# Kernel tuning notes

Measured on AMD Instinct MI355X. Metric: run time of the kernel, lower is better.

## Reference

```python
import jax, jax.numpy as jnp
import numpy as np

B, S, D, H = 2, 4096, 512, 8
DK = D // H  # 64

def setup_inputs() -> dict:
    key = jax.random.key(0)
    k1, k2, k3, k4 = jax.random.split(key, 4)
    return {
        "queries": jax.random.normal(k1, (B, S, D), dtype=jnp.float32),
        "keys": jax.random.normal(k2, (B, S, D), dtype=jnp.float32),
        "values": jax.random.normal(k3, (B, S, D), dtype=jnp.float32),
        "W_o": jax.random.normal(k4, (D, D), dtype=jnp.float32) * (1.0 / np.sqrt(D)),
        "b_o": jnp.zeros((D,), dtype=jnp.float32),
    }

def reference(queries, keys, values, W_o, b_o):
    b_s, nq, _ = queries.shape
    nk = keys.shape[1]
    # split heads: (b, s, h, dk) -> (b, h, s, dk)
    q = queries.reshape(b_s, nq, H, DK).transpose(0, 2, 1, 3)
    k = keys.reshape(b_s, nk, H, DK).transpose(0, 2, 1, 3)
    v = values.reshape(b_s, nk, H, DK).transpose(0, 2, 1, 3)
    # full (nq, nk) attention matrix, scaled by sqrt(d_k)
    att = jnp.einsum("bhqd,bhkd->bhqk", q, k) / np.sqrt(DK).astype(np.float32)
    att = jax.nn.softmax(att, axis=-1)  # dropout is identity at inference
    out = jnp.einsum("bhqk,bhkd->bhqd", att, v)
    out = out.transpose(0, 2, 1, 3).reshape(b_s, nq, H * DK)
    return out @ W_o + b_o
```

## Files before the change

kernel.cpp:

```cpp
#include <hip/hip_runtime.h>
#include <hip/hip_bf16.h>

#define Bn 2
#define Sn 4096
#define Dn 512
#define Hn 8

typedef _Float16 f16x8 __attribute__((ext_vector_type(8)));
typedef __fp16 fp16x2 __attribute__((ext_vector_type(2)));
typedef float f32x16 __attribute__((ext_vector_type(16)));
typedef unsigned uint2v __attribute__((ext_vector_type(2)));

#if __has_builtin(__builtin_amdgcn_global_load_lds)
#define HAS_GLL 1
typedef const __attribute__((address_space(1))) unsigned int* gas1_t;
typedef __attribute__((address_space(3))) unsigned int* las3_t;
static __device__ __forceinline__ void ld_lds16(const void* g, void* l) {
    __builtin_amdgcn_global_load_lds((gas1_t)g, (las3_t)l, 16, 0, 0);
}
#else
#define HAS_GLL 0
#endif

static __device__ __forceinline__ unsigned pkh(float a, float b) {
    union { fp16x2 h; unsigned u; } r;
    r.h = __builtin_amdgcn_cvt_pkrtz(a, b);
    return r.u;
}

static __device__ __forceinline__ f16x8 xchg2(unsigned g0x, unsigned g0y,
                                              unsigned g1x, unsigned g1y, int hi) {
    union { unsigned u[4]; f16x8 v; } f;
#if __has_builtin(__builtin_amdgcn_permlane32_swap)
    uint2v rx = __builtin_amdgcn_permlane32_swap(g0x, g1x, false, false);
    uint2v ry = __builtin_amdgcn_permlane32_swap(g0y, g1y, false, false);
    f.u[0] = rx.x; f.u[1] = ry.x; f.u[2] = rx.y; f.u[3] = ry.y;
#else
    int sx = hi ? (int)g0x : (int)g1x;
    int sy = hi ? (int)g0y : (int)g1y;
    int rx = __shfl_xor(sx, 32);
    int ry = __shfl_xor(sy, 32);
    unsigned ox = hi ? g1x : g0x;
    unsigned oy = hi ? g1y : g0y;
    f.u[0] = hi ? (unsigned)rx : ox;
    f.u[1] = hi ? (unsigned)ry : oy;
    f.u[2] = hi ? ox : (unsigned)rx;
    f.u[3] = hi ? oy : (unsigned)ry;
#endif
    return f.v;
}

__global__ __launch_bounds__(256) void prep_kernel(
    const float* __restrict__ K, const float* __restrict__ V, const float* __restrict__ W,
    unsigned short* __restrict__ Kb, unsigned short* __restrict__ Vb,
    unsigned short* __restrict__ Wb) {
    const int vb = blockIdx.x;
    const int tid = threadIdx.x;
    if (vb < 1024) {
        const int kt = vb & 63, bh = vb >> 6;
        const int b = bh >> 3, h = bh & 7;
        unsigned short* dst = Kb + ((size_t)bh * 64 + kt) * 4096;
#pragma unroll
        for (int i = 0; i < 2; ++i) {
            int c = tid + i * 256;
            int f = c >> 6, ln = c & 63;
            int ktile = f >> 2, ks = f & 3;
            int row = ktile * 32 + (ln & 31);
            int dk = ks * 16 + (ln >> 5) * 8;
            const float* src = K + ((size_t)(b * Sn + kt * 64 + row)) * Dn + h * 64 + dk;
            float4 a0 = *(const float4*)src;
            float4 a1 = *(const float4*)(src + 4);
            uint4 o;
            o.x = pkh(a0.x, a0.y); o.y = pkh(a0.z, a0.w);
            o.z = pkh(a1.x, a1.y); o.w = pkh(a1.z, a1.w);
            *(uint4*)(dst + c * 8) = o;
        }
    } else if (vb < 2048) {
        const int u = vb - 1024;
        const int kt = u & 63, bh = u >> 6;
        const int b = bh >> 3, h = bh & 7;
        unsigned short* dst = Vb + ((size_t)bh * 64 + kt) * 4096;
#pragma unroll
        for (int i = 0; i < 2; ++i) {
            int c = tid + i * 256;
            int f = c >> 6, ln = c & 63;
            int dt = f >> 2, ks = f & 3;
            int dk = dt * 32 + (ln & 31);
            int key0 = ks * 16 + (ln >> 5) * 8;
            const float* src = V + ((size_t)(b * Sn + kt * 64 + key0)) * Dn + h * 64 + dk;
            uint4 o;
            o.x = pkh(src[0 * Dn], src[1 * Dn]);
            o.y = pkh(src[2 * Dn], src[3 * Dn]);
            o.z = pkh(src[4 * Dn], src[5 * Dn]);
            o.w = pkh(src[6 * Dn], src[7 * Dn]);
            *(uint4*)(dst + c * 8) = o;
        }
    } else {
        int c = (vb - 2048) * 256 + tid;
        int ln = c & 63, f = c >> 6;
        int ntile = f >> 5, ks = f & 31;
        int n = ntile * 32 + (ln & 31);
        int k0 = ks * 16 + (ln >> 5) * 8;
        uint4 o;
        o.x = pkh(W[(size_t)(k0 + 0) * Dn + n], W[(size_t)(k0 + 1) * Dn + n]);
        o.y = pkh(W[(size_t)(k0 + 2) * Dn + n], W[(size_t)(k0 + 3) * Dn + n]);
        o.z = pkh(W[(size_t)(k0 + 4) * Dn + n], W[(size_t)(k0 + 5) * Dn + n]);
        o.w = pkh(W[(size_t)(k0 + 6) * Dn + n], W[(size_t)(k0 + 7) * Dn + n]);
        *(uint4*)(Wb + c * 8) = o;
    }
}

__global__ __launch_bounds__(512, 2) void attn_kernel(
    const float* __restrict__ Q,
    const unsigned short* __restrict__ Kb,
    const unsigned short* __restrict__ Vb,
    unsigned short* __restrict__ ObA) {
    __shared__ __align__(16) unsigned short KV[32768];

    const int id = blockIdx.x + (blockIdx.y << 5);
    const int qt = (id >> 3) & 31;
    const int bh = (id & 7) + ((id >> 8) << 3);
    const int b = bh >> 3, h = bh & 7;
    const int tid = threadIdx.x;
    const int wg = tid >> 6;
    const int kg = wg >> 1;
    const int qs = wg & 1;
    const int lane = tid & 63;
    const int q = lane & 31;
    const int hi = lane >> 5;
    const float cexp = 0.18033688f;

    f16x8 qf0[4], qf1[4];
    {
        const float* qp0 = Q + ((size_t)(b * Sn + qt * 128 + qs * 64 + q)) * Dn + h * 64 + hi * 8;
        const float* qp1 = qp0 + (size_t)32 * Dn;
#pragma unroll
        for (int ks = 0; ks < 4; ++ks) {
            float4 a0 = *(const float4*)(qp0 + ks * 16);
            float4 a1 = *(const float4*)(qp0 + ks * 16 + 4);
            union { unsigned u[4]; f16x8 v; } f;
            f.u[0] = pkh(a0.x * cexp, a0.y * cexp);
            f.u[1] = pkh(a0.z * cexp, a0.w * cexp);
            f.u[2] = pkh(a1.x * cexp, a1.y * cexp);
            f.u[3] = pkh(a1.z * cexp, a1.w * cexp);
            qf0[ks] = f.v;
            a0 = *(const float4*)(qp1 + ks * 16);
            a1 = *(const float4*)(qp1 + ks * 16 + 4);
            f.u[0] = pkh(a0.x * cexp, a0.y * cexp);
            f.u[1] = pkh(a0.z * cexp, a0.w * cexp);
            f.u[2] = pkh(a1.x * cexp, a1.y * cexp);
            f.u[3] = pkh(a1.z * cexp, a1.w * cexp);
            qf1[ks] = f.v;
        }
    }

    f32x16 zf;
#pragma unroll
    for (int r = 0; r < 16; ++r) zf[r] = 0.f;
    f32x16 oacc[2][2];
    oacc[0][0] = zf; oacc[0][1] = zf; oacc[1][0] = zf; oacc[1][1] = zf;
    float l0_ = 0.f, l1_ = 0.f;

    const size_t bhbase = (size_t)bh * 64 * 4096;

#if HAS_GLL
#define STAGE(itx, bb) { \
    const int t64 = kg * 16 + ((itx) >> 1); \
    const int lohi = (itx) & 1; \
    unsigned short* dst = &KV[(bb) * 16384 + kg * 4096]; \
    if (qs == 0) { \
        const unsigned short* sp = Kb + bhbase + (size_t)t64 * 4096 + lohi * 2048 + lane * 8; \
        ld_lds16(sp, dst); ld_lds16(sp + 512, dst + 512); \
        ld_lds16(sp + 1024, dst + 1024); ld_lds16(sp + 1536, dst + 1536); \
    } else { \
        const unsigned short* sp = Vb + bhbase + (size_t)t64 * 4096 + lohi * 1024 + lane * 8; \
        unsigned short* dv = dst + 2048; \
        ld_lds16(sp, dv); ld_lds16(sp + 512, dv + 512); \
        ld_lds16(sp + 2048, dv + 1024); ld_lds16(sp + 2560, dv + 1536); \
    } }
#else
#define STAGE(itx, bb) { \
    const int t64 = kg * 16 + ((itx) >> 1); \
    const int lohi = (itx) & 1; \
    unsigned short* dst = &KV[(bb) * 16384 + kg * 4096]; \
    if (qs == 0) { \
        const unsigned short* sp = Kb + bhbase + (size_t)t64 * 4096 + lohi * 2048 + lane * 8; \
        uint4 a0 = *(const uint4*)(sp); uint4 a1 = *(const uint4*)(sp + 512); \
        uint4 a2 = *(const uint4*)(sp + 1024); uint4 a3 = *(const uint4*)(sp + 1536); \
        *(uint4*)&dst[lane * 8] = a0; *(uint4*)&dst[512 + lane * 8] = a1; \
        *(uint4*)&dst[1024 + lane * 8] = a2; *(uint4*)&dst[1536 + lane * 8] = a3; \
    } else { \
        const unsigned short* sp = Vb + bhbase + (size_t)t64 * 4096 + lohi * 1024 + lane * 8; \
        unsigned short* dv = dst + 2048; \
        uint4 a0 = *(const uint4*)(sp); uint4 a1 = *(const uint4*)(sp + 512); \
        uint4 a2 = *(const uint4*)(sp + 2048); uint4 a3 = *(const uint4*)(sp + 2560); \
        *(uint4*)&dv[lane * 8] = a0; *(uint4*)&dv[512 + lane * 8] = a1; \
        *(uint4*)&dv[1024 + lane * 8] = a2; *(uint4*)&dv[1536 + lane * 8] = a3; \
    } }
#endif

    STAGE(0, 0);

    for (int it = 0; it < 32; ++it) {
        __syncthreads();
        const unsigned short* Kbuf = &KV[(it & 1) * 16384 + kg * 4096];
        const unsigned short* Vbuf = Kbuf + 2048;
        if (it < 31) STAGE(it + 1, (it + 1) & 1);

        f32x16 sa0, sa1;
        {
            f16x8 kf = *(const f16x8*)&Kbuf[0 * 512 + lane * 8];
            sa0 = __builtin_amdgcn_mfma_f32_32x32x16_f16(kf, qf0[0], zf, 0, 0, 0);
            sa1 = __builtin_amdgcn_mfma_f32_32x32x16_f16(kf, qf1[0], zf, 0, 0, 0);
#pragma unroll
            for (int ks = 1; ks < 4; ++ks) {
                kf = *(const f16x8*)&Kbuf[ks * 512 + lane * 8];
                sa0 = __builtin_amdgcn_mfma_f32_32x32x16_f16(kf, qf0[ks], sa0, 0, 0, 0);
                sa1 = __builtin_amdgcn_mfma_f32_32x32x16_f16(kf, qf1[ks], sa1, 0, 0, 0);
            }
        }
        unsigned u0[8], u1[8];
        float s0 = 0.f, s1 = 0.f;
#pragma unroll
        for (int j = 0; j < 8; ++j) {
            float ea = __builtin_amdgcn_exp2f(sa0[2 * j]);
            float eb = __builtin_amdgcn_exp2f(sa0[2 * j + 1]);
            s0 += ea + eb;
            u0[j] = pkh(ea, eb);
        }
#pragma unroll
        for (int j = 0; j < 8; ++j) {
            float ea = __builtin_amdgcn_exp2f(sa1[2 * j]);
            float eb = __builtin_amdgcn_exp2f(sa1[2 * j + 1]);
            s1 += ea + eb;
            u1[j] = pkh(ea, eb);
        }
        l0_ += s0; l1_ += s1;

#pragma unroll
        for (int ks2 = 0; ks2 < 2; ++ks2) {
            f16x8 pb0 = xchg2(u0[4 * ks2 + 0], u0[4 * ks2 + 1], u0[4 * ks2 + 2], u0[4 * ks2 + 3], hi);
            f16x8 pb1 = xchg2(u1[4 * ks2 + 0], u1[4 * ks2 + 1], u1[4 * ks2 + 2], u1[4 * ks2 + 3], hi);
            f16x8 va0 = *(const f16x8*)&Vbuf[ks2 * 512 + lane * 8];
            f16x8 va1 = *(const f16x8*)&Vbuf[1024 + ks2 * 512 + lane * 8];
            oacc[0][0] = __builtin_amdgcn_mfma_f32_32x32x16_f16(va0, pb0, oacc[0][0], 0, 0, 0);
            oacc[0][1] = __builtin_amdgcn_mfma_f32_32x32x16_f16(va1, pb0, oacc[0][1], 0, 0, 0);
            oacc[1][0] = __builtin_amdgcn_mfma_f32_32x32x16_f16(va0, pb1, oacc[1][0], 0, 0, 0);
            oacc[1][1] = __builtin_amdgcn_mfma_f32_32x32x16_f16(va1, pb1, oacc[1][1], 0, 0, 0);
        }
    }

    __syncthreads();
    float* red = (float*)KV;
#pragma unroll
    for (int t = 0; t < 2; ++t) {
        if (kg != 0) {
            float* rp = red + (qs * 3 + (kg - 1)) * 2048;
#pragma unroll
            for (int dt = 0; dt < 2; ++dt)
#pragma unroll
                for (int g = 0; g < 4; ++g) {
                    float4 v;
                    v.x = oacc[t][dt][g * 4 + 0];
                    v.y = oacc[t][dt][g * 4 + 1];
                    v.z = oacc[t][dt][g * 4 + 2];
                    v.w = oacc[t][dt][g * 4 + 3];
                    *(float4*)&rp[(dt * 4 + g) * 256 + lane * 4] = v;
                }
            red[12288 + (qs * 3 + (kg - 1)) * 64 + lane] = t ? l1_ : l0_;
        }
        __syncthreads();
        if (kg == 0) {
#pragma unroll
            for (int slot = 0; slot < 3; ++slot) {
                float* rp = red + (qs * 3 + slot) * 2048;
#pragma unroll
                for (int dt = 0; dt < 2; ++dt)
#pragma unroll
                    for (int g = 0; g < 4; ++g) {
                        float4 v = *(const float4*)&rp[(dt * 4 + g) * 256 + lane * 4];
                        oacc[t][dt][g * 4 + 0] += v.x;
                        oacc[t][dt][g * 4 + 1] += v.y;
                        oacc[t][dt][g * 4 + 2] += v.z;
                        oacc[t][dt][g * 4 + 3] += v.w;
                    }
                float addl = red[12288 + (qs * 3 + slot) * 64 + lane];
                if (t) l1_ += addl; else l0_ += addl;
            }
        }
        __syncthreads();
    }

    if (kg == 0) {
        l0_ += __shfl_xor(l0_, 32);
        l1_ += __shfl_xor(l1_, 32);
#pragma unroll
        for (int t = 0; t < 2; ++t) {
            const float li = 1.f / (t ? l1_ : l0_);
            const int gm = b * 128 + qt * 4 + qs * 2 + t;
#pragma unroll
            for (int ksg = 0; ksg < 4; ++ksg) {
                const int dt = ksg >> 1, k2 = ksg & 1;
                unsigned g0x = pkh(oacc[t][dt][8 * k2 + 0] * li, oacc[t][dt][8 * k2 + 1] * li);
                unsigned g0y = pkh(oacc[t][dt][8 * k2 + 2] * li, oacc[t][dt][8 * k2 + 3] * li);
                unsigned g1x = pkh(oacc[t][dt][8 * k2 + 4] * li, oacc[t][dt][8 * k2 + 5] * li);
                unsigned g1y = pkh(oacc[t][dt][8 * k2 + 6] * li, oacc[t][dt][8 * k2 + 7] * li);
                f16x8 frag = xchg2(g0x, g0y, g1x, g1y, hi);
                union { f16x8 v; uint4 u; } fu; fu.v = frag;
                *(uint4*)&ObA[((size_t)(gm * 32 + h * 4 + ksg) * 64 + lane) * 8] = fu.u;
            }
        }
    }
}

__global__ __launch_bounds__(256) void proj_kernel(
    const unsigned short* __restrict__ ObA,
    const unsigned short* __restrict__ Wb,
    const float* __restrict__ bias,
    float* __restrict__ out) {
    __shared__ __align__(16) unsigned short Ash[8192];
    __shared__ __align__(16) unsigned short Wsh[4096];

    const int mt = blockIdx.x;
    const int nt = blockIdx.y;
    const int tid = threadIdx.x;
    const int w = tid >> 6;
    const int lane = tid & 63;
    const int q = lane & 31;
    const int hi = lane >> 5;

    f32x16 acc[2];
#pragma unroll
    for (int t = 0; t < 2; ++t)
#pragma unroll
        for (int r = 0; r < 16; ++r) acc[t][r] = 0.f;

    for (int kt = 0; kt < 8; ++kt) {
        __syncthreads();
#pragma unroll
        for (int i = 0; i < 4; ++i) {
            int ci = (tid >> 6) + i * 4;
            int ml = ci >> 2, ksl = ci & 3;
            *(uint4*)&Ash[ci * 512 + lane * 8] =
                *(const uint4*)(ObA + (((size_t)(mt * 4 + ml) * 32 + kt * 4 + ksl) * 64 + lane) * 8);
        }
#pragma unroll
        for (int i = 0; i < 2; ++i) {
            int ci = (tid >> 6) + i * 4;
            int ntl = ci >> 2, ksl = ci & 3;
            *(uint4*)&Wsh[ci * 512 + lane * 8] =
                *(const uint4*)(Wb + (((size_t)(nt * 2 + ntl) * 32 + kt * 4 + ksl) * 64 + lane) * 8);
        }
        __syncthreads();

#pragma unroll
        for (int ks = 0; ks < 4; ++ks) {
            f16x8 a  = *(const f16x8*)&Ash[(w * 4 + ks) * 512 + lane * 8];
            f16x8 b0 = *(const f16x8*)&Wsh[(0 * 4 + ks) * 512 + lane * 8];
            f16x8 b1 = *(const f16x8*)&Wsh[(4 + ks) * 512 + lane * 8];
            acc[0] = __builtin_amdgcn_mfma_f32_32x32x16_f16(a, b0, acc[0], 0, 0, 0);
            acc[1] = __builtin_amdgcn_mfma_f32_32x32x16_f16(a, b1, acc[1], 0, 0, 0);
        }
    }

#pragma unroll
    for (int ntl = 0; ntl < 2; ++ntl) {
        int col = nt * 64 + ntl * 32 + q;
        float bv = bias[col];
#pragma unroll
        for (int reg = 0; reg < 16; ++reg) {
            int row = mt * 128 + w * 32 + (reg & 3) + 8 * (reg >> 2) + 4 * hi;
            out[(size_t)row * Dn + col] = acc[ntl][reg] + bv;
        }
    }
}

extern "C" void kernel_launch(void* const* d_in, const int* in_sizes, int n_in,
                              void* d_out, int out_size, void* d_ws, size_t ws_size,
                              hipStream_t stream) {
    const float* Q = (const float*)d_in[0];
    const float* K = (const float*)d_in[1];
    const float* V = (const float*)d_in[2];
    const float* W = (const float*)d_in[3];
    const float* bo = (const float*)d_in[4];
    float* out = (float*)d_out;

    char* ws = (char*)d_ws;
    unsigned short* Kb  = (unsigned short*)(ws);
    unsigned short* Vb  = (unsigned short*)(ws + 8388608);
    unsigned short* Wb  = (unsigned short*)(ws + 16777216);
    unsigned short* ObA = (unsigned short*)(ws + 17301504);

    prep_kernel<<<2176, 256, 0, stream>>>(K, V, W, Kb, Vb, Wb);
    attn_kernel<<<dim3(32, 16), 512, 0, stream>>>(Q, Kb, Vb, ObA);
    proj_kernel<<<dim3(64, 8), 256, 0, stream>>>(ObA, Wb, bo, out);
}
```

Baseline: 188.6 us.

## Shrink attention blocks to 4 waves with per-wave private K/V staging, no block barriers

Each attention block now has 256 threads and covers 64 queries instead of 128, with twice as many blocks. Each wave loads its own K and V chunk into a private LDS slice and waits on its own loads, so the per-iteration __syncthreads and double buffering are gone. LDS per block is halved, which allows more resident blocks per CU. The cost is that loads are no longer overlapped with compute inside a wave, and every K/V tile is read by twice as many blocks overall.

```diff
diff --git a/kernel.cpp b/kernel.cpp
--- a/kernel.cpp
+++ b/kernel.cpp
@@ -110,21 +110,19 @@
     }
 }
 
-__global__ __launch_bounds__(512, 2) void attn_kernel(
+__global__ __launch_bounds__(256, 4) void attn_kernel(
     const float* __restrict__ Q,
     const unsigned short* __restrict__ Kb,
     const unsigned short* __restrict__ Vb,
     unsigned short* __restrict__ ObA) {
-    __shared__ __align__(16) unsigned short KV[32768];
-
-    const int id = blockIdx.x + (blockIdx.y << 5);
-    const int qt = (id >> 3) & 31;
-    const int bh = (id & 7) + ((id >> 8) << 3);
+    __shared__ __align__(16) unsigned short KV[16384];
+
+    const int id = blockIdx.x + (blockIdx.y << 6);
+    const int qt = (id >> 3) & 63;
+    const int bh = (id & 7) + ((id >> 9) << 3);
     const int b = bh >> 3, h = bh & 7;
     const int tid = threadIdx.x;
-    const int wg = tid >> 6;
-    const int kg = wg >> 1;
-    const int qs = wg & 1;
+    const int kg = tid >> 6;
     const int lane = tid & 63;
     const int q = lane & 31;
     const int hi = lane >> 5;
@@ -132,7 +130,7 @@
 
     f16x8 qf0[4], qf1[4];
     {
-        const float* qp0 = Q + ((size_t)(b * Sn + qt * 128 + qs * 64 + q)) * Dn + h * 64 + hi * 8;
+        const float* qp0 = Q + ((size_t)(b * Sn + qt * 64 + q)) * Dn + h * 64 + hi * 8;
         const float* qp1 = qp0 + (size_t)32 * Dn;
 #pragma unroll
         for (int ks = 0; ks < 4; ++ks) {
@@ -162,59 +160,46 @@
     float l0_ = 0.f, l1_ = 0.f;
 
     const size_t bhbase = (size_t)bh * 64 * 4096;
-
+    const unsigned short* kB = Kb + bhbase;
+    const unsigned short* vB = Vb + bhbase;
+    unsigned short* const lb = &KV[kg * 4096];
+
+    for (int it = 0; it < 32; ++it) {
+        const int t64 = kg * 16 + (it >> 1);
+        const int lohi = it & 1;
+        {
+            const unsigned short* ks_ = kB + (size_t)t64 * 4096 + lohi * 2048 + lane * 8;
+            const unsigned short* vs_ = vB + (size_t)t64 * 4096 + lohi * 1024 + lane * 8;
 #if HAS_GLL
-#define STAGE(itx, bb) { \
-    const int t64 = kg * 16 + ((itx) >> 1); \
-    const int lohi = (itx) & 1; \
-    unsigned short* dst = &KV[(bb) * 16384 + kg * 4096]; \
-    if (qs == 0) { \
-        const unsigned short* sp = Kb + bhbase + (size_t)t64 * 4096 + lohi * 2048 + lane * 8; \
-        ld_lds16(sp, dst); ld_lds16(sp + 512, dst + 512); \
-        ld_lds16(sp + 1024, dst + 1024); ld_lds16(sp + 1536, dst + 1536); \
-    } else { \
-        const unsigned short* sp = Vb + bhbase + (size_t)t64 * 4096 + lohi * 1024 + lane * 8; \
-        unsigned short* dv = dst + 2048; \
-        ld_lds16(sp, dv); ld_lds16(sp + 512, dv + 512); \
-        ld_lds16(sp + 2048, dv + 1024); ld_lds16(sp + 2560, dv + 1536); \
-    } }
+            ld_lds16(ks_, lb);          ld_lds16(ks_ + 512, lb + 512);
+            ld_lds16(ks_ + 1024, lb + 1024); ld_lds16(ks_ + 1536, lb + 1536);
+            ld_lds16(vs_, lb + 2048);   ld_lds16(vs_ + 512, lb + 2560);
+            ld_lds16(vs_ + 2048, lb + 3072); ld_lds16(vs_ + 2560, lb + 3584);
+            asm volatile("s_waitcnt vmcnt(0)" ::: "memory");
 #else
-#define STAGE(itx, bb) { \
-    const int t64 = kg * 16 + ((itx) >> 1); \
-    const int lohi = (itx) & 1; \
-    unsigned short* dst = &KV[(bb) * 16384 + kg * 4096]; \
-    if (qs == 0) { \
-        const unsigned short* sp = Kb + bhbase + (size_t)t64 * 4096 + lohi * 2048 + lane * 8; \
-        uint4 a0 = *(const uint4*)(sp); uint4 a1 = *(const uint4*)(sp + 512); \
-        uint4 a2 = *(const uint4*)(sp + 1024); uint4 a3 = *(const uint4*)(sp + 1536); \
-        *(uint4*)&dst[lane * 8] = a0; *(uint4*)&dst[512 + lane * 8] = a1; \
-        *(uint4*)&dst[1024 + lane * 8] = a2; *(uint4*)&dst[1536 + lane * 8] = a3; \
-    } else { \
-        const unsigned short* sp = Vb + bhbase + (size_t)t64 * 4096 + lohi * 1024 + lane * 8; \
-        unsigned short* dv = dst + 2048; \
-        uint4 a0 = *(const uint4*)(sp); uint4 a1 = *(const uint4*)(sp + 512); \
-        uint4 a2 = *(const uint4*)(sp + 2048); uint4 a3 = *(const uint4*)(sp + 2560); \
-        *(uint4*)&dv[lane * 8] = a0; *(uint4*)&dv[512 + lane * 8] = a1; \
-        *(uint4*)&dv[1024 + lane * 8] = a2; *(uint4*)&dv[1536 + lane * 8] = a3; \
-    } }
+            uint4 a0 = *(const uint4*)(ks_);        uint4 a1 = *(const uint4*)(ks_ + 512);
+            uint4 a2 = *(const uint4*)(ks_ + 1024); uint4 a3 = *(const uint4*)(ks_ + 1536);
+            uint4 b0 = *(const uint4*)(vs_);        uint4 b1 = *(const uint4*)(vs_ + 512);
+            uint4 b2 = *(const uint4*)(vs_ + 2048); uint4 b3 = *(const uint4*)(vs_ + 2560);
+            *(uint4*)&lb[lane * 8] = a0;        *(uint4*)&lb[512 + lane * 8] = a1;
+            *(uint4*)&lb[1024 + lane * 8] = a2; *(uint4*)&lb[1536 + lane * 8] = a3;
+            *(uint4*)&lb[2048 + lane * 8] = b0; *(uint4*)&lb[2560 + lane * 8] = b1;
+            *(uint4*)&lb[3072 + lane * 8] = b2; *(uint4*)&lb[3584 + lane * 8] = b3;
+            asm volatile("s_waitcnt lgkmcnt(0)" ::: "memory");
 #endif
-
-    STAGE(0, 0);
-
-    for (int it = 0; it < 32; ++it) {
-        __syncthreads();
-        const unsigned short* Kbuf = &KV[(it & 1) * 16384 + kg * 4096];
-        const unsigned short* Vbuf = Kbuf + 2048;
-        if (it < 31) STAGE(it + 1, (it + 1) & 1);
+#if __has_builtin(__builtin_amdgcn_sched_barrier)
+            __builtin_amdgcn_sched_barrier(0);
+#endif
+        }
 
         f32x16 sa0, sa1;
         {
-            f16x8 kf = *(const f16x8*)&Kbuf[0 * 512 + lane * 8];
+            f16x8 kf = *(const f16x8*)&lb[0 * 512 + lane * 8];
             sa0 = __builtin_amdgcn_mfma_f32_32x32x16_f16(kf, qf0[0], zf, 0, 0, 0);
             sa1 = __builtin_amdgcn_mfma_f32_32x32x16_f16(kf, qf1[0], zf, 0, 0, 0);
 #pragma unroll
             for (int ks = 1; ks < 4; ++ks) {
-                kf = *(const f16x8*)&Kbuf[ks * 512 + lane * 8];
+                kf = *(const f16x8*)&lb[ks * 512 + lane * 8];
                 sa0 = __builtin_amdgcn_mfma_f32_32x32x16_f16(kf, qf0[ks], sa0, 0, 0, 0);
                 sa1 = __builtin_amdgcn_mfma_f32_32x32x16_f16(kf, qf1[ks], sa1, 0, 0, 0);
             }
@@ -241,8 +226,8 @@
         for (int ks2 = 0; ks2 < 2; ++ks2) {
             f16x8 pb0 = xchg2(u0[4 * ks2 + 0], u0[4 * ks2 + 1], u0[4 * ks2 + 2], u0[4 * ks2 + 3], hi);
             f16x8 pb1 = xchg2(u1[4 * ks2 + 0], u1[4 * ks2 + 1], u1[4 * ks2 + 2], u1[4 * ks2 + 3], hi);
-            f16x8 va0 = *(const f16x8*)&Vbuf[ks2 * 512 + lane * 8];
-            f16x8 va1 = *(const f16x8*)&Vbuf[1024 + ks2 * 512 + lane * 8];
+            f16x8 va0 = *(const f16x8*)&lb[2048 + ks2 * 512 + lane * 8];
+            f16x8 va1 = *(const f16x8*)&lb[3072 + ks2 * 512 + lane * 8];
             oacc[0][0] = __builtin_amdgcn_mfma_f32_32x32x16_f16(va0, pb0, oacc[0][0], 0, 0, 0);
             oacc[0][1] = __builtin_amdgcn_mfma_f32_32x32x16_f16(va1, pb0, oacc[0][1], 0, 0, 0);
             oacc[1][0] = __builtin_amdgcn_mfma_f32_32x32x16_f16(va0, pb1, oacc[1][0], 0, 0, 0);
@@ -255,7 +240,7 @@
 #pragma unroll
     for (int t = 0; t < 2; ++t) {
         if (kg != 0) {
-            float* rp = red + (qs * 3 + (kg - 1)) * 2048;
+            float* rp = red + (kg - 1) * 2048;
 #pragma unroll
             for (int dt = 0; dt < 2; ++dt)
 #pragma unroll
@@ -267,13 +252,13 @@
                     v.w = oacc[t][dt][g * 4 + 3];
                     *(float4*)&rp[(dt * 4 + g) * 256 + lane * 4] = v;
                 }
-            red[12288 + (qs * 3 + (kg - 1)) * 64 + lane] = t ? l1_ : l0_;
+            red[6144 + (kg - 1) * 64 + lane] = t ? l1_ : l0_;
         }
         __syncthreads();
         if (kg == 0) {
 #pragma unroll
             for (int slot = 0; slot < 3; ++slot) {
-                float* rp = red + (qs * 3 + slot) * 2048;
+                float* rp = red + slot * 2048;
 #pragma unroll
                 for (int dt = 0; dt < 2; ++dt)
 #pragma unroll
@@ -284,7 +269,7 @@
                         oacc[t][dt][g * 4 + 2] += v.z;
                         oacc[t][dt][g * 4 + 3] += v.w;
                     }
-                float addl = red[12288 + (qs * 3 + slot) * 64 + lane];
+                float addl = red[6144 + slot * 64 + lane];
                 if (t) l1_ += addl; else l0_ += addl;
             }
         }
@@ -297,7 +282,7 @@
 #pragma unroll
         for (int t = 0; t < 2; ++t) {
             const float li = 1.f / (t ? l1_ : l0_);
-            const int gm = b * 128 + qt * 4 + qs * 2 + t;
+            const int gm = b * 128 + qt * 2 + t;
 #pragma unroll
             for (int ksg = 0; ksg < 4; ++ksg) {
                 const int dt = ksg >> 1, k2 = ksg & 1;
@@ -392,6 +377,6 @@
     unsigned short* ObA = (unsigned short*)(ws + 17301504);
 
     prep_kernel<<<2176, 256, 0, stream>>>(K, V, W, Kb, Vb, Wb);
-    attn_kernel<<<dim3(32, 16), 512, 0, stream>>>(Q, Kb, Vb, ObA);
+    attn_kernel<<<dim3(64, 16), 256, 0, stream>>>(Q, Kb, Vb, ObA);
     proj_kernel<<<dim3(64, 8), 256, 0, stream>>>(ObA, Wb, bo, out);
 }
```

After: 337.1 us. 78.7% more time.
